# Kernel optimization log

Hardware: AMD Instinct MI355X
Metric: run time of the kernel (lower is better)

## Reference

```python
import jax, jax.numpy as jnp
import numpy as np

B, L, S = 8192, 1024, 3
OUTSIDE, TM_HELIX, INSIDE = 0, 1, 2


def setup_inputs() -> dict:
    key = jax.random.key(0)
    k1, k2 = jax.random.split(key)
    emissions = jax.random.normal(k1, (B, L, S), dtype=jnp.float32)
    tags = jax.random.randint(k2, (B, L), 0, S)
    mask = jnp.ones((B, L), dtype=jnp.float32)
    t = np.zeros((S, S), dtype=np.float32)
    t[OUTSIDE, INSIDE] = -5.0
    t[INSIDE, OUTSIDE] = -5.0
    t[OUTSIDE, TM_HELIX] = 1.0
    t[INSIDE, TM_HELIX] = 1.0
    t[TM_HELIX, OUTSIDE] = 1.0
    t[TM_HELIX, INSIDE] = 1.0
    transitions = jnp.asarray(t)
    return {"emissions": emissions, "mask": mask, "transitions": transitions, "tags": tags}


def _score_sentence(emissions, tags, mask, transitions):
    # emission score of the gold tag at every position: (B, L)
    em_score = jnp.take_along_axis(emissions, tags[..., None], axis=2)[..., 0]
    # transition score between consecutive gold tags: (B, L-1)
    trans_score = transitions[tags[:, :-1], tags[:, 1:]]
    return em_score[:, 0] * mask[:, 0] + jnp.sum(
        (trans_score + em_score[:, 1:]) * mask[:, 1:], axis=1
    )


def _forward_alg(emissions, mask, transitions):
    def step(alpha, xs):
        em_t, m_t = xs  # (B, S), (B,)
        # scores[b, i, j] = alpha[b, i] + T[i, j] + em_t[b, j]
        scores = alpha[:, :, None] + transitions[None, :, :] + em_t[:, None, :]
        new_alpha = jax.nn.logsumexp(scores, axis=1)
        alpha = jnp.where(m_t[:, None] > 0, new_alpha, alpha)
        return alpha, None

    alpha0 = emissions[:, 0, :]
    xs = (jnp.swapaxes(emissions[:, 1:, :], 0, 1),  # (L-1, B, S)
          jnp.swapaxes(mask[:, 1:], 0, 1))          # (L-1, B)
    alpha, _ = jax.lax.scan(step, alpha0, xs)
    return jax.nn.logsumexp(alpha, axis=1)  # (B,)


def reference(emissions, mask, transitions, tags):
    logZ = _forward_alg(emissions, mask, transitions)
    gold = _score_sentence(emissions, tags, mask, transitions)
    return jnp.mean(logZ - gold)
```

## Files before the change

kernel.cpp:

```cpp
#include <hip/hip_runtime.h>


#define LOG2E 1.4426950408889634f
#define LN2   0.6931471805599453f

constexpr int B = 8192;
constexpr int L = 1024;
constexpr int S = 3;
constexpr int CHUNK = 16;
constexpr int SEQS_PER_BLOCK = 4;

__device__ __forceinline__ float fast_exp2(float x) { return __builtin_amdgcn_exp2f(x); }
__device__ __forceinline__ float fast_log2(float x) { return __builtin_amdgcn_logf(x); }

__device__ __forceinline__ void matmul3(float* __restrict__ D,
                                        const float* __restrict__ A,
                                        const float* __restrict__ Bm) {
  #pragma unroll
  for (int i = 0; i < 3; ++i)
    #pragma unroll
    for (int j = 0; j < 3; ++j)
      D[i * 3 + j] = A[i * 3 + 0] * Bm[0 * 3 + j] +
                     A[i * 3 + 1] * Bm[1 * 3 + j] +
                     A[i * 3 + 2] * Bm[2 * 3 + j];
}

__device__ __forceinline__ void renorm3(float* __restrict__ P, float& scale) {
  float m = P[0];
  #pragma unroll
  for (int e = 1; e < 9; ++e) m = fmaxf(m, P[e]);
  int ex;
  (void)frexpf(m, &ex);
  #pragma unroll
  for (int e = 0; e < 9; ++e) P[e] = ldexpf(P[e], -ex);
  scale += (float)ex;
}

__global__ __launch_bounds__(256) void crf_main(
    const float* __restrict__ em, const float* __restrict__ mask,
    const float* __restrict__ trans, const int* __restrict__ tags,
    float* __restrict__ ws) {
  const int lane = threadIdx.x & 63;
  const int b = blockIdx.x * SEQS_PER_BLOCK + (threadIdx.x >> 6);

  float T2[9], tk[9];
  #pragma unroll
  for (int e = 0; e < 9; ++e) {
    T2[e] = trans[e] * LOG2E;
    tk[e] = fast_exp2(T2[e]);
  }

  const float4* em4 = (const float4*)(em + (size_t)b * (L * S));
  float ev[CHUNK * 3];
  #pragma unroll
  for (int u = 0; u < 12; ++u) {
    float4 v = em4[lane * 12 + u];
    ev[4 * u + 0] = v.x * LOG2E;
    ev[4 * u + 1] = v.y * LOG2E;
    ev[4 * u + 2] = v.z * LOG2E;
    ev[4 * u + 3] = v.w * LOG2E;
  }
  const float4* mk4 = (const float4*)(mask + (size_t)b * L);
  float mk[CHUNK];
  #pragma unroll
  for (int u = 0; u < 4; ++u) {
    float4 v = mk4[lane * 4 + u];
    mk[4 * u + 0] = v.x; mk[4 * u + 1] = v.y;
    mk[4 * u + 2] = v.z; mk[4 * u + 3] = v.w;
  }
  const int4* tg4 = (const int4*)(tags + (size_t)b * L);
  int tg[CHUNK];
  #pragma unroll
  for (int u = 0; u < 4; ++u) {
    int4 v = tg4[lane * 4 + u];
    tg[4 * u + 0] = v.x; tg[4 * u + 1] = v.y;
    tg[4 * u + 2] = v.z; tg[4 * u + 3] = v.w;
  }

  int prev = __shfl_up(tg[CHUNK - 1], 1);
  float gold = 0.f;
  #pragma unroll
  for (int s = 0; s < CHUNK; ++s) {
    const int cur = tg[s];
    const float e = (cur == 0) ? ev[s * 3 + 0]
                   : ((cur == 1) ? ev[s * 3 + 1] : ev[s * 3 + 2]);
    if (s == 0 && lane == 0) {
      gold = e * mk[0];
    } else {
      const float r0 = (cur == 0) ? T2[0] : ((cur == 1) ? T2[1] : T2[2]);
      const float r1 = (cur == 0) ? T2[3] : ((cur == 1) ? T2[4] : T2[5]);
      const float r2 = (cur == 0) ? T2[6] : ((cur == 1) ? T2[7] : T2[8]);
      const float tr = (prev == 0) ? r0 : ((prev == 1) ? r1 : r2);
      gold += (tr + e) * mk[s];
    }
    prev = cur;
  }
  #pragma unroll
  for (int d = 1; d < 64; d <<= 1) gold += __shfl_xor(gold, d, 64);

  float P[9] = {1.f, 0.f, 0.f, 0.f, 1.f, 0.f, 0.f, 0.f, 1.f};
  float scale = 0.f;
  #pragma unroll
  for (int s = 0; s < CHUNK; ++s) {
    const bool doStep = (mk[s] > 0.f) && !(s == 0 && lane == 0);
    if (doStep) {
      const float w0 = fast_exp2(ev[s * 3 + 0]);
      const float w1 = fast_exp2(ev[s * 3 + 1]);
      const float w2 = fast_exp2(ev[s * 3 + 2]);
      float M[9] = {tk[0] * w0, tk[1] * w1, tk[2] * w2,
                    tk[3] * w0, tk[4] * w1, tk[5] * w2,
                    tk[6] * w0, tk[7] * w1, tk[8] * w2};
      float N[9];
      matmul3(N, P, M);
      #pragma unroll
      for (int e = 0; e < 9; ++e) P[e] = N[e];
    }
    if (s == 7) renorm3(P, scale);
  }
  renorm3(P, scale);

  #pragma unroll
  for (int d = 1; d < 64; d <<= 1) {
    float o[9];
    #pragma unroll
    for (int e = 0; e < 9; ++e) o[e] = __shfl_xor(P[e], d, 64);
    const float osc = __shfl_xor(scale, d, 64);
    const bool later = (lane & d) != 0;
    float A[9], Bm[9];
    #pragma unroll
    for (int e = 0; e < 9; ++e) {
      A[e]  = later ? o[e] : P[e];
      Bm[e] = later ? P[e] : o[e];
    }
    float N[9];
    matmul3(N, A, Bm);
    #pragma unroll
    for (int e = 0; e < 9; ++e) P[e] = N[e];
    scale += osc;
    renorm3(P, scale);
  }

  if (lane == 0) {
    const float a0 = fast_exp2(ev[0]);
    const float a1 = fast_exp2(ev[1]);
    const float a2 = fast_exp2(ev[2]);
    const float z = a0 * (P[0] + P[1] + P[2]) +
                    a1 * (P[3] + P[4] + P[5]) +
                    a2 * (P[6] + P[7] + P[8]);
    const float logZ2 = scale + fast_log2(z);
    ws[b] = LN2 * (logZ2 - gold);
  }
}

__global__ __launch_bounds__(256) void crf_reduce(const float* __restrict__ ws,
                                                  float* __restrict__ out) {
  __shared__ float red[4];
  const int tid = threadIdx.x;
  float s = 0.f;
  for (int i = tid; i < B; i += 256) s += ws[i];
  #pragma unroll
  for (int d = 1; d < 64; d <<= 1) s += __shfl_xor(s, d, 64);
  if ((tid & 63) == 0) red[tid >> 6] = s;
  __syncthreads();
  if (tid == 0) out[0] = (red[0] + red[1] + red[2] + red[3]) * (1.0f / (float)B);
}

extern "C" void kernel_launch(void* const* d_in, const int* in_sizes, int n_in,
                              void* d_out, int out_size, void* d_ws, size_t ws_size,
                              hipStream_t stream) {
  const float* em    = (const float*)d_in[0];
  const float* mask  = (const float*)d_in[1];
  const float* trans = (const float*)d_in[2];
  const int*   tags  = (const int*)d_in[3];
  float* ws  = (float*)d_ws;
  float* out = (float*)d_out;

  crf_main<<<B / SEQS_PER_BLOCK, 256, 0, stream>>>(em, mask, trans, tags, ws);
  crf_reduce<<<1, 256, 0, stream>>>(ws, out);
}
```

Baseline: 204.2 us.

## Fuse final reduction via atomics and interleave loads with scan compute

Removes the separate reduce kernel: each block sums its per-sequence losses in shared memory and atomically adds into the output, which is zeroed by a memset. The per-lane loads are split into groups so the gold-score and matrix-product work can start before all data arrives, and masked steps become selects instead of branches. Renormalisation is dropped inside the cross-lane scan and launch bounds now request higher occupancy. The atomic float sum is order-dependent, and skipping renorm in the shuffle combine risks overflow for long products.

```diff
diff --git a/kernel.cpp b/kernel.cpp
--- a/kernel.cpp
+++ b/kernel.cpp
@@ -6,12 +6,20 @@
 
 constexpr int B = 8192;
 constexpr int L = 1024;
-constexpr int S = 3;
-constexpr int CHUNK = 16;
 constexpr int SEQS_PER_BLOCK = 4;
 
-__device__ __forceinline__ float fast_exp2(float x) { return __builtin_amdgcn_exp2f(x); }
-__device__ __forceinline__ float fast_log2(float x) { return __builtin_amdgcn_logf(x); }
+__device__ __forceinline__ float fexp2(float x) { return __builtin_amdgcn_exp2f(x); }
+__device__ __forceinline__ float flog2(float x) { return __builtin_amdgcn_logf(x); }
+
+__device__ __forceinline__ float mux3(float x0, float x1, float x2, int i) {
+  return (i == 0) ? x0 : ((i == 1) ? x1 : x2);
+}
+__device__ __forceinline__ float trmux(const float* __restrict__ T2, int p, int c) {
+  const float r0 = mux3(T2[0], T2[1], T2[2], c);
+  const float r1 = mux3(T2[3], T2[4], T2[5], c);
+  const float r2 = mux3(T2[6], T2[7], T2[8], c);
+  return mux3(r0, r1, r2, p);
+}
 
 __device__ __forceinline__ void matmul3(float* __restrict__ D,
                                         const float* __restrict__ A,
@@ -36,88 +44,82 @@
   scale += (float)ex;
 }
 
-__global__ __launch_bounds__(256) void crf_main(
+__global__ __launch_bounds__(256, 4) void crf_main(
     const float* __restrict__ em, const float* __restrict__ mask,
     const float* __restrict__ trans, const int* __restrict__ tags,
-    float* __restrict__ ws) {
+    float* __restrict__ out) {
   const int lane = threadIdx.x & 63;
-  const int b = blockIdx.x * SEQS_PER_BLOCK + (threadIdx.x >> 6);
+  const int wid = threadIdx.x >> 6;
+  const int b = blockIdx.x * SEQS_PER_BLOCK + wid;
 
   float T2[9], tk[9];
   #pragma unroll
   for (int e = 0; e < 9; ++e) {
     T2[e] = trans[e] * LOG2E;
-    tk[e] = fast_exp2(T2[e]);
+    tk[e] = fexp2(T2[e]);
   }
 
-  const float4* em4 = (const float4*)(em + (size_t)b * (L * S));
-  float ev[CHUNK * 3];
-  #pragma unroll
-  for (int u = 0; u < 12; ++u) {
-    float4 v = em4[lane * 12 + u];
-    ev[4 * u + 0] = v.x * LOG2E;
-    ev[4 * u + 1] = v.y * LOG2E;
-    ev[4 * u + 2] = v.z * LOG2E;
-    ev[4 * u + 3] = v.w * LOG2E;
-  }
+  const float4* em4 = (const float4*)(em + (size_t)b * (L * 3));
   const float4* mk4 = (const float4*)(mask + (size_t)b * L);
-  float mk[CHUNK];
-  #pragma unroll
-  for (int u = 0; u < 4; ++u) {
-    float4 v = mk4[lane * 4 + u];
-    mk[4 * u + 0] = v.x; mk[4 * u + 1] = v.y;
-    mk[4 * u + 2] = v.z; mk[4 * u + 3] = v.w;
-  }
-  const int4* tg4 = (const int4*)(tags + (size_t)b * L);
-  int tg[CHUNK];
-  #pragma unroll
-  for (int u = 0; u < 4; ++u) {
-    int4 v = tg4[lane * 4 + u];
-    tg[4 * u + 0] = v.x; tg[4 * u + 1] = v.y;
-    tg[4 * u + 2] = v.z; tg[4 * u + 3] = v.w;
-  }
-
-  int prev = __shfl_up(tg[CHUNK - 1], 1);
-  float gold = 0.f;
-  #pragma unroll
-  for (int s = 0; s < CHUNK; ++s) {
-    const int cur = tg[s];
-    const float e = (cur == 0) ? ev[s * 3 + 0]
-                   : ((cur == 1) ? ev[s * 3 + 1] : ev[s * 3 + 2]);
-    if (s == 0 && lane == 0) {
-      gold = e * mk[0];
-    } else {
-      const float r0 = (cur == 0) ? T2[0] : ((cur == 1) ? T2[1] : T2[2]);
-      const float r1 = (cur == 0) ? T2[3] : ((cur == 1) ? T2[4] : T2[5]);
-      const float r2 = (cur == 0) ? T2[6] : ((cur == 1) ? T2[7] : T2[8]);
-      const float tr = (prev == 0) ? r0 : ((prev == 1) ? r1 : r2);
-      gold += (tr + e) * mk[s];
-    }
-    prev = cur;
-  }
-  #pragma unroll
-  for (int d = 1; d < 64; d <<= 1) gold += __shfl_xor(gold, d, 64);
+  const int4*   tg4 = (const int4*)(tags + (size_t)b * L);
 
   float P[9] = {1.f, 0.f, 0.f, 0.f, 1.f, 0.f, 0.f, 0.f, 1.f};
-  float scale = 0.f;
+  float scale = 0.f, gold = 0.f;
+  float a0 = 0.f, a1 = 0.f, a2 = 0.f;
+  float e0_sel = 0.f, mk0 = 0.f;
+  int tag0 = 0, prev = 0;
+
   #pragma unroll
-  for (int s = 0; s < CHUNK; ++s) {
-    const bool doStep = (mk[s] > 0.f) && !(s == 0 && lane == 0);
-    if (doStep) {
-      const float w0 = fast_exp2(ev[s * 3 + 0]);
-      const float w1 = fast_exp2(ev[s * 3 + 1]);
-      const float w2 = fast_exp2(ev[s * 3 + 2]);
-      float M[9] = {tk[0] * w0, tk[1] * w1, tk[2] * w2,
-                    tk[3] * w0, tk[4] * w1, tk[5] * w2,
-                    tk[6] * w0, tk[7] * w1, tk[8] * w2};
+  for (int g = 0; g < 4; ++g) {
+    const float4 x0 = em4[lane * 12 + 3 * g + 0];
+    const float4 x1 = em4[lane * 12 + 3 * g + 1];
+    const float4 x2 = em4[lane * 12 + 3 * g + 2];
+    const float4 mm = mk4[lane * 4 + g];
+    const int4   tt = tg4[lane * 4 + g];
+    const float ef[12] = {x0.x, x0.y, x0.z, x0.w, x1.x, x1.y, x1.z, x1.w,
+                          x2.x, x2.y, x2.z, x2.w};
+    const float mf[4] = {mm.x, mm.y, mm.z, mm.w};
+    const int   tf[4] = {tt.x, tt.y, tt.z, tt.w};
+
+    #pragma unroll
+    for (int j = 0; j < 4; ++j) {
+      const int s = 4 * g + j;
+      const float ev0 = ef[3 * j + 0] * LOG2E;
+      const float ev1 = ef[3 * j + 1] * LOG2E;
+      const float ev2 = ef[3 * j + 2] * LOG2E;
+      const float m = mf[j];
+      const int cur = tf[j];
+
+      const float e = mux3(ev0, ev1, ev2, cur);
+      if (s == 0) {
+        e0_sel = e; mk0 = m; tag0 = cur;
+      } else {
+        gold = fmaf(trmux(T2, prev, cur) + e, m, gold);
+      }
+      prev = cur;
+
+      const float w0 = fexp2(ev0);
+      const float w1 = fexp2(ev1);
+      const float w2 = fexp2(ev2);
+      if (s == 0) { a0 = w0; a1 = w1; a2 = w2; }
+      const bool act = (m > 0.f) && !(s == 0 && lane == 0);
+      const float M[9] = {tk[0] * w0, tk[1] * w1, tk[2] * w2,
+                          tk[3] * w0, tk[4] * w1, tk[5] * w2,
+                          tk[6] * w0, tk[7] * w1, tk[8] * w2};
       float N[9];
       matmul3(N, P, M);
       #pragma unroll
-      for (int e = 0; e < 9; ++e) P[e] = N[e];
+      for (int e2 = 0; e2 < 9; ++e2) P[e2] = act ? N[e2] : P[e2];
+
+      if (s == 7 || s == 15) renorm3(P, scale);
     }
-    if (s == 7) renorm3(P, scale);
   }
-  renorm3(P, scale);
+
+  const int prevLast = __shfl_up(prev, 1);
+  if (lane == 0) gold = fmaf(e0_sel, mk0, gold);
+  else           gold = fmaf(trmux(T2, prevLast, tag0) + e0_sel, mk0, gold);
+  #pragma unroll
+  for (int d = 1; d < 64; d <<= 1) gold += __shfl_xor(gold, d, 64);
 
   #pragma unroll
   for (int d = 1; d < 64; d <<= 1) {
@@ -137,32 +139,20 @@
     #pragma unroll
     for (int e = 0; e < 9; ++e) P[e] = N[e];
     scale += osc;
-    renorm3(P, scale);
   }
 
+  __shared__ float red[SEQS_PER_BLOCK];
   if (lane == 0) {
-    const float a0 = fast_exp2(ev[0]);
-    const float a1 = fast_exp2(ev[1]);
-    const float a2 = fast_exp2(ev[2]);
     const float z = a0 * (P[0] + P[1] + P[2]) +
                     a1 * (P[3] + P[4] + P[5]) +
                     a2 * (P[6] + P[7] + P[8]);
-    const float logZ2 = scale + fast_log2(z);
-    ws[b] = LN2 * (logZ2 - gold);
+    red[wid] = LN2 * (scale + flog2(z) - gold);
   }
-}
-
-__global__ __launch_bounds__(256) void crf_reduce(const float* __restrict__ ws,
-                                                  float* __restrict__ out) {
-  __shared__ float red[4];
-  const int tid = threadIdx.x;
-  float s = 0.f;
-  for (int i = tid; i < B; i += 256) s += ws[i];
-  #pragma unroll
-  for (int d = 1; d < 64; d <<= 1) s += __shfl_xor(s, d, 64);
-  if ((tid & 63) == 0) red[tid >> 6] = s;
   __syncthreads();
-  if (tid == 0) out[0] = (red[0] + red[1] + red[2] + red[3]) * (1.0f / (float)B);
+  if (threadIdx.x == 0) {
+    const float s = red[0] + red[1] + red[2] + red[3];
+    atomicAdd(out, s * (1.0f / (float)B));
+  }
 }
 
 extern "C" void kernel_launch(void* const* d_in, const int* in_sizes, int n_in,
@@ -172,9 +162,8 @@
   const float* mask  = (const float*)d_in[1];
   const float* trans = (const float*)d_in[2];
   const int*   tags  = (const int*)d_in[3];
-  float* ws  = (float*)d_ws;
   float* out = (float*)d_out;
 
-  crf_main<<<B / SEQS_PER_BLOCK, 256, 0, stream>>>(em, mask, trans, tags, ws);
-  crf_reduce<<<1, 256, 0, stream>>>(ws, out);
+  hipMemsetAsync(out, 0, sizeof(float), stream);
+  crf_main<<<B / SEQS_PER_BLOCK, 256, 0, stream>>>(em, mask, trans, tags, out);
 }
```

New measurement: 197.2 us. 3.5% less time.
